# Kernel tuning notes

Hardware: AMD Instinct MI355X
Metric: run time of the kernel (lower is better)

The kernel has to match this reference:

```python
import jax, jax.numpy as jnp
import numpy as np

N = 100000   # num nodes
E = 1600000  # num edges (before self-loops)
D_IN, D_HID, D_OUT = 128, 128, 64


def _gcn_layer(x, W, b, src, dst, norm):
    # GCNConv: h = x @ W, then normalized sparse aggregation, then bias.
    h = x @ W                              # [N, d_out]
    msg = h[src] * norm[:, None]           # [E+N, d_out] gathered + scaled messages
    out = jax.ops.segment_sum(msg, dst, num_segments=N)  # scatter-add to dst nodes
    return out + b


def reference(x, W1, b1, W2, b2, edge_index):
    src0, dst0 = edge_index[0], edge_index[1]
    # GCNConv adds self-loops by default
    loop = jnp.arange(N, dtype=src0.dtype)
    src = jnp.concatenate([src0, loop])
    dst = jnp.concatenate([dst0, loop])
    # symmetric normalization: deg^{-1/2}[src] * deg^{-1/2}[dst]
    deg = jax.ops.segment_sum(jnp.ones_like(src, dtype=x.dtype), dst, num_segments=N)
    dinv = jnp.where(deg > 0, jax.lax.rsqrt(jnp.maximum(deg, 1.0)), 0.0)
    norm = dinv[src] * dinv[dst]           # [E+N]

    h = jax.nn.relu(_gcn_layer(x, W1, b1, src, dst, norm))
    return _gcn_layer(h, W2, b2, src, dst, norm)


def setup_inputs() -> dict:
    key = jax.random.key(0)
    k1, k2, k3, k4 = jax.random.split(key, 4)
    x = jax.random.normal(k1, (N, D_IN), dtype=jnp.float32)
    # glorot-ish init for weights
    W1 = jax.random.normal(k2, (D_IN, D_HID), dtype=jnp.float32) * (1.0 / np.sqrt(D_IN))
    b1 = jnp.zeros((D_HID,), dtype=jnp.float32)
    W2 = jax.random.normal(k3, (D_HID, D_OUT), dtype=jnp.float32) * (1.0 / np.sqrt(D_HID))
    b2 = jnp.zeros((D_OUT,), dtype=jnp.float32)
    edge_index = jax.random.randint(k4, (2, E), 0, N, dtype=jnp.int64)
    return {"x": x, "W1": W1, "b1": b1, "W2": W2, "b2": b2, "edge_index": edge_index}
```

## Files before the change

kernel.cpp:

```cpp
#include <hip/hip_runtime.h>

static constexpr int NN = 100000;
static constexpr int EE = 1600000;
static constexpr int BSZ = 64;
static constexpr int NB = (NN + BSZ - 1) / BSZ;
static constexpr int BCAP = 2048;
static constexpr int TILE = 2048;


__device__ __forceinline__ unsigned short f2bf(float f) {
    unsigned u = __float_as_uint(f);
    u += 0x7FFFu + ((u >> 16) & 1u);
    return (unsigned short)(u >> 16);
}
__device__ __forceinline__ float bfl(unsigned u) { return __uint_as_float(u << 16); }
__device__ __forceinline__ float bfh(unsigned u) { return __uint_as_float(u & 0xFFFF0000u); }

typedef __attribute__((ext_vector_type(8))) short short8;
typedef __attribute__((ext_vector_type(4))) float float4v;


__global__ __launch_bounds__(256) void k_init(const float* __restrict__ W1,
                                              const float* __restrict__ W2,
                                              unsigned short* __restrict__ W1t,
                                              unsigned short* __restrict__ W2t,
                                              int* __restrict__ bcur) {
    int idx = blockIdx.x * 256 + threadIdx.x;
    if (idx < 16384) {
        int n = idx >> 7, k = idx & 127;
        W1t[idx] = f2bf(W1[k * 128 + n]);
    } else if (idx < 24576) {
        int j = idx - 16384;
        int n = j >> 7, k = j & 127;
        W2t[j] = f2bf(W2[k * 64 + n]);
    } else if (idx < 24576 + NB) {
        int b = idx - 24576;
        bcur[b] = b * BCAP;
    }
}


__global__ __launch_bounds__(256) void k_bin(const int* __restrict__ src,
                                             const int* __restrict__ dst,
                                             int* __restrict__ bcur,
                                             int* __restrict__ ebuf, int E) {
    constexpr int K = TILE / 256;
    __shared__ int lcnt[NB];
    __shared__ int lbase[NB];
    const int t = threadIdx.x;
    const int e0 = blockIdx.x * TILE;

    for (int i = t; i < NB; i += 256) lcnt[i] = 0;
    __syncthreads();

    int dreg[K], ofs[K];
#pragma unroll
    for (int k = 0; k < K; ++k) {
        int e = e0 + k * 256 + t;
        if (e < E) {
            int d = dst[e];
            dreg[k] = d;
            ofs[k] = atomicAdd(&lcnt[d >> 6], 1);
        } else dreg[k] = -1;
    }
    __syncthreads();

    for (int i = t; i < NB; i += 256) {
        int c = lcnt[i];
        lbase[i] = c ? atomicAdd(&bcur[i], c) : 0;
    }
    __syncthreads();

#pragma unroll
    for (int k = 0; k < K; ++k) {
        if (dreg[k] >= 0) {
            int e = e0 + k * 256 + t;
            int s = src[e];
            int b = dreg[k] >> 6;
            ebuf[lbase[b] + ofs[k]] = (s << 6) | (dreg[k] & 63);
        }
    }
}


__global__ __launch_bounds__(256) void k_csr(const int* __restrict__ bcur,
                                             const int* __restrict__ ebuf,
                                             int* __restrict__ rowbeg,
                                             int* __restrict__ rowend,
                                             float* __restrict__ dinv,
                                             int* __restrict__ csr, int n) {
    __shared__ int lcnt[BSZ];
    __shared__ int lofs[BSZ];
    const int b = blockIdx.x, t = threadIdx.x;
    if (t < BSZ) lcnt[t] = 0;
    __syncthreads();
    const int beg = b * BCAP, end = bcur[b];
    for (int j = beg + t; j < end; j += 256) atomicAdd(&lcnt[ebuf[j] & 63], 1);
    __syncthreads();
    if (t < BSZ) {
        int c = lcnt[t];
        int x = c;
#pragma unroll
        for (int off = 1; off < 64; off <<= 1) {
            int y = __shfl_up(x, off, 64);
            if (t >= off) x += y;
        }
        int exc = x - c;
        int node = b * BSZ + t;
        if (node < n) {
            rowbeg[node] = beg + exc;
            rowend[node] = beg + exc + c;
            dinv[node] = rsqrtf((float)c + 1.0f);
        }
        lofs[t] = beg + exc;
    }
    __syncthreads();
    for (int j = beg + t; j < end; j += 256) {
        int e = ebuf[j];
        int pos = atomicAdd(&lofs[e & 63], 1);
        csr[pos] = e >> 6;
    }
}


__global__ __launch_bounds__(256) void k_gemm128m(const float* __restrict__ X,
                                                  const unsigned short* __restrict__ W1t,
                                                  const float* __restrict__ dinv,
                                                  unsigned* __restrict__ G, int M) {
    __shared__ float cls[4 * 16 * 132];
    const int t = threadIdx.x;
    const int w = t >> 6, lane = t & 63;
    const int quad = lane >> 4, m16 = lane & 15;
    const int row0 = blockIdx.x * 64 + w * 16;
    int arow = row0 + m16; if (arow >= M) arow = M - 1;

    short8 afrag[4];
#pragma unroll
    for (int ks = 0; ks < 4; ++ks) {
        const float* p = X + (size_t)arow * 128 + ks * 32 + quad * 8;
        float4 u0 = ((const float4*)p)[0];
        float4 u1 = ((const float4*)p)[1];
        short8 a;
        a[0] = (short)f2bf(u0.x); a[1] = (short)f2bf(u0.y);
        a[2] = (short)f2bf(u0.z); a[3] = (short)f2bf(u0.w);
        a[4] = (short)f2bf(u1.x); a[5] = (short)f2bf(u1.y);
        a[6] = (short)f2bf(u1.z); a[7] = (short)f2bf(u1.w);
        afrag[ks] = a;
    }
    float* myc = cls + w * 16 * 132;
#pragma unroll
    for (int nt = 0; nt < 8; ++nt) {
        float4v acc = {0.f, 0.f, 0.f, 0.f};
#pragma unroll
        for (int ks = 0; ks < 4; ++ks) {
            const short8 b = *((const short8*)(W1t + (size_t)(nt * 16 + m16) * 128 + ks * 32 + quad * 8));
            acc = __builtin_amdgcn_mfma_f32_16x16x32_bf16(afrag[ks], b, acc, 0, 0, 0);
        }
#pragma unroll
        for (int r = 0; r < 4; ++r)
            myc[(quad * 4 + r) * 132 + nt * 16 + m16] = acc[r];
    }
    __syncthreads();
#pragma unroll
    for (int i = 0; i < 8; ++i) {
        int idx = i * 64 + lane;
        int r = idx >> 5, c = idx & 31;
        int grow = row0 + r;
        if (grow < M) {
            float4 v = *((const float4*)(myc + r * 132 + c * 4));
            float s = dinv[grow];
            uint2 p;
            p.x = (unsigned)f2bf(v.x * s) | ((unsigned)f2bf(v.y * s) << 16);
            p.y = (unsigned)f2bf(v.z * s) | ((unsigned)f2bf(v.w * s) << 16);
            ((uint2*)G)[(size_t)grow * 32 + c] = p;
        }
    }
}


__global__ __launch_bounds__(256) void k_gemm64m(const unsigned short* __restrict__ X,
                                                 const unsigned short* __restrict__ W2t,
                                                 const float* __restrict__ dinv,
                                                 unsigned* __restrict__ G, int M) {
    __shared__ float cls[4 * 16 * 68];
    const int t = threadIdx.x;
    const int w = t >> 6, lane = t & 63;
    const int quad = lane >> 4, m16 = lane & 15;
    const int row0 = blockIdx.x * 64 + w * 16;
    int arow = row0 + m16; if (arow >= M) arow = M - 1;

    short8 afrag[4];
#pragma unroll
    for (int ks = 0; ks < 4; ++ks)
        afrag[ks] = *((const short8*)(X + (size_t)arow * 128 + ks * 32 + quad * 8));

    float* myc = cls + w * 16 * 68;
#pragma unroll
    for (int nt = 0; nt < 4; ++nt) {
        float4v acc = {0.f, 0.f, 0.f, 0.f};
#pragma unroll
        for (int ks = 0; ks < 4; ++ks) {
            const short8 b = *((const short8*)(W2t + (size_t)(nt * 16 + m16) * 128 + ks * 32 + quad * 8));
            acc = __builtin_amdgcn_mfma_f32_16x16x32_bf16(afrag[ks], b, acc, 0, 0, 0);
        }
#pragma unroll
        for (int r = 0; r < 4; ++r)
            myc[(quad * 4 + r) * 68 + nt * 16 + m16] = acc[r];
    }
    __syncthreads();
#pragma unroll
    for (int i = 0; i < 4; ++i) {
        int idx = i * 64 + lane;
        int r = idx >> 4, c = idx & 15;
        int grow = row0 + r;
        if (grow < M) {
            float4 v = *((const float4*)(myc + r * 68 + c * 4));
            float s = dinv[grow];
            uint2 p;
            p.x = (unsigned)f2bf(v.x * s) | ((unsigned)f2bf(v.y * s) << 16);
            p.y = (unsigned)f2bf(v.z * s) | ((unsigned)f2bf(v.w * s) << 16);
            ((uint2*)G)[(size_t)grow * 16 + c] = p;
        }
    }
}


__global__ __launch_bounds__(256) void k_gather128(const int* __restrict__ rowbeg,
                                                   const int* __restrict__ rowend,
                                                   const int* __restrict__ csr,
                                                   const unsigned* __restrict__ G,
                                                   const float* __restrict__ dinv,
                                                   const float* __restrict__ bias,
                                                   unsigned* __restrict__ OUT,
                                                   int n, int nwaves) {
    const int wid = blockIdx.x * 4 + (threadIdx.x >> 6);
    const int lane = threadIdx.x & 63;
    const int sub = lane & 31;
    const int half = lane >> 5;
    for (int node = wid; node < n; node += nwaves) {
        const int beg = rowbeg[node];
        const int end = rowend[node];
        float a0 = 0.f, a1 = 0.f, a2 = 0.f, a3 = 0.f;
        for (int c = beg; c < end; c += 64) {
            int ec = end - c; if (ec > 64) ec = 64;
            const int idx = csr[c + ((lane < ec) ? lane : 0)];
            int pb = 0;
            for (; pb + 16 <= ec; pb += 16) {
#pragma unroll
                for (int q = 0; q < 8; ++q) {
                    int s = __shfl(idx, pb + 2 * q + half, 64);
                    uint2 v = *((const uint2*)(G + (size_t)s * 64 + 2 * sub));
                    a0 += bfl(v.x); a1 += bfh(v.x); a2 += bfl(v.y); a3 += bfh(v.y);
                }
            }
            if (pb < ec) {
#pragma unroll
                for (int q = 0; q < 8; ++q) {
                    int e = pb + 2 * q + half;
                    bool valid = e < ec;
                    int s = __shfl(idx, valid ? e : 0, 64);
                    uint2 v = *((const uint2*)(G + (size_t)s * 64 + 2 * sub));
                    if (valid) { a0 += bfl(v.x); a1 += bfh(v.x); a2 += bfl(v.y); a3 += bfh(v.y); }
                }
            }
        }
        a0 += __shfl_xor(a0, 32, 64);
        a1 += __shfl_xor(a1, 32, 64);
        a2 += __shfl_xor(a2, 32, 64);
        a3 += __shfl_xor(a3, 32, 64);
        if (half == 0) {
            uint2 vs = *((const uint2*)(G + (size_t)node * 64 + 2 * sub));
            a0 += bfl(vs.x); a1 += bfh(vs.x); a2 += bfl(vs.y); a3 += bfh(vs.y);
            const float di = dinv[node];
            const float4 bv = ((const float4*)bias)[sub];
            float r0 = fmaf(a0, di, bv.x), r1 = fmaf(a1, di, bv.y);
            float r2 = fmaf(a2, di, bv.z), r3 = fmaf(a3, di, bv.w);
            r0 = fmaxf(r0, 0.f); r1 = fmaxf(r1, 0.f);
            r2 = fmaxf(r2, 0.f); r3 = fmaxf(r3, 0.f);
            uint2 p;
            p.x = (unsigned)f2bf(r0) | ((unsigned)f2bf(r1) << 16);
            p.y = (unsigned)f2bf(r2) | ((unsigned)f2bf(r3) << 16);
            ((uint2*)OUT)[(size_t)node * 32 + sub] = p;
        }
    }
}


__global__ __launch_bounds__(256) void k_gather64(const int* __restrict__ rowbeg,
                                                  const int* __restrict__ rowend,
                                                  const int* __restrict__ csr,
                                                  const unsigned* __restrict__ G,
                                                  const float* __restrict__ dinv,
                                                  const float* __restrict__ bias,
                                                  float* __restrict__ OUT,
                                                  int n, int nwaves) {
    const int wid = blockIdx.x * 4 + (threadIdx.x >> 6);
    const int lane = threadIdx.x & 63;
    const int sub = lane & 15;
    const int qh = lane >> 4;
    for (int node = wid; node < n; node += nwaves) {
        const int beg = rowbeg[node];
        const int end = rowend[node];
        float a0 = 0.f, a1 = 0.f, a2 = 0.f, a3 = 0.f;
        for (int c = beg; c < end; c += 64) {
            int ec = end - c; if (ec > 64) ec = 64;
            const int idx = csr[c + ((lane < ec) ? lane : 0)];
            int pb = 0;
            for (; pb + 32 <= ec; pb += 32) {
#pragma unroll
                for (int q = 0; q < 8; ++q) {
                    int s = __shfl(idx, pb + 4 * q + qh, 64);
                    uint2 v = ((const uint2*)(G + (size_t)s * 32))[sub];
                    a0 += bfl(v.x); a1 += bfh(v.x); a2 += bfl(v.y); a3 += bfh(v.y);
                }
            }
            if (pb < ec) {
#pragma unroll
                for (int q = 0; q < 8; ++q) {
                    int e = pb + 4 * q + qh;
                    bool valid = e < ec;
                    int s = __shfl(idx, valid ? e : 0, 64);
                    uint2 v = ((const uint2*)(G + (size_t)s * 32))[sub];
                    if (valid) { a0 += bfl(v.x); a1 += bfh(v.x); a2 += bfl(v.y); a3 += bfh(v.y); }
                }
            }
        }
        a0 += __shfl_xor(a0, 16, 64); a0 += __shfl_xor(a0, 32, 64);
        a1 += __shfl_xor(a1, 16, 64); a1 += __shfl_xor(a1, 32, 64);
        a2 += __shfl_xor(a2, 16, 64); a2 += __shfl_xor(a2, 32, 64);
        a3 += __shfl_xor(a3, 16, 64); a3 += __shfl_xor(a3, 32, 64);
        if (qh == 0) {
            uint2 vs = ((const uint2*)(G + (size_t)node * 32))[sub];
            a0 += bfl(vs.x); a1 += bfh(vs.x); a2 += bfl(vs.y); a3 += bfh(vs.y);
            const float di = dinv[node];
            const float4 bv = ((const float4*)bias)[sub];
            float4 r;
            r.x = fmaf(a0, di, bv.x);
            r.y = fmaf(a1, di, bv.y);
            r.z = fmaf(a2, di, bv.z);
            r.w = fmaf(a3, di, bv.w);
            ((float4*)OUT)[(size_t)node * 16 + sub] = r;
        }
    }
}


extern "C" void kernel_launch(void* const* d_in, const int* in_sizes, int n_in,
                              void* d_out, int out_size, void* d_ws, size_t ws_size,
                              hipStream_t stream) {
    const float* x  = (const float*)d_in[0];
    const float* W1 = (const float*)d_in[1];
    const float* b1 = (const float*)d_in[2];
    const float* W2 = (const float*)d_in[3];
    const float* b2 = (const float*)d_in[4];
    const int*   ei = (const int*)d_in[5];
    const int* src = ei;
    const int* dst = ei + EE;
    float* out = (float*)d_out;

    int*   bcur   = (int*)d_ws;
    float* dinv   = (float*)(bcur + NB);
    int*   rowbeg = (int*)(dinv + NN);
    int*   rowend = rowbeg + NN;
    int*   ebuf   = rowend + NN;
    int*   csr    = ebuf + (size_t)NB * BCAP;
    unsigned* g1b = (unsigned*)(csr + (size_t)NB * BCAP);
    unsigned* h1b = g1b + (size_t)NN * 64;
    unsigned* g2b = h1b + (size_t)NN * 64;
    unsigned short* w1t = (unsigned short*)(g2b + (size_t)NN * 32);
    unsigned short* w2t = w1t + 16384;

    constexpr int GB = 2048;
    constexpr int NW = GB * 4;
    constexpr int IB = (24576 + NB + 255) / 256;

    k_init<<<IB, 256, 0, stream>>>(W1, W2, w1t, w2t, bcur);
    k_bin<<<(EE + TILE - 1) / TILE, 256, 0, stream>>>(src, dst, bcur, ebuf, EE);
    k_csr<<<NB, 256, 0, stream>>>(bcur, ebuf, rowbeg, rowend, dinv, csr, NN);

    k_gemm128m<<<(NN + 63) / 64, 256, 0, stream>>>(x, w1t, dinv, g1b, NN);
    k_gather128<<<GB, 256, 0, stream>>>(rowbeg, rowend, csr, g1b, dinv, b1, h1b, NN, NW);

    k_gemm64m<<<(NN + 63) / 64, 256, 0, stream>>>((const unsigned short*)h1b, w2t, dinv, g2b, NN);
    k_gather64<<<GB, 256, 0, stream>>>(rowbeg, rowend, csr, g2b, dinv, b2, out, NN, NW);
}
```

Measured before the change: 345.6 us.

## Slice feature matrices into column slabs and gather per slab for cache locality

Intermediate feature matrices G1, H1 and G2 are stored as column slabs of 16 features (NN x 16 bf16 each), and the GEMM epilogues and A-operand loads are rewritten to match. A single templated gather kernel assigns blocks to one slab, so each wave gathers 32-byte rows from a slab small enough to stay in cache, with 4 nodes per wave and 16 edges per step. Row begin and end are packed into an int2, with nontemporal loads and stores and software prefetch of the next node's CSR indices. The cost is that the csr list is read once per slice (8 or 4 times), plus more complex indexing.

```diff
diff --git a/kernel.cpp b/kernel.cpp
--- a/kernel.cpp
+++ b/kernel.cpp
@@ -6,6 +6,7 @@
 static constexpr int NB = (NN + BSZ - 1) / BSZ;
 static constexpr int BCAP = 2048;
 static constexpr int TILE = 2048;
+static constexpr int GB = 2048;
 
 
 __device__ __forceinline__ unsigned short f2bf(float f) {
@@ -18,6 +19,7 @@
 
 typedef __attribute__((ext_vector_type(8))) short short8;
 typedef __attribute__((ext_vector_type(4))) float float4v;
+typedef __attribute__((ext_vector_type(4))) float float4n;
 
 
 __global__ __launch_bounds__(256) void k_init(const float* __restrict__ W1,
@@ -85,8 +87,7 @@
 
 __global__ __launch_bounds__(256) void k_csr(const int* __restrict__ bcur,
                                              const int* __restrict__ ebuf,
-                                             int* __restrict__ rowbeg,
-                                             int* __restrict__ rowend,
+                                             int2* __restrict__ rbe,
                                              float* __restrict__ dinv,
                                              int* __restrict__ csr, int n) {
     __shared__ int lcnt[BSZ];
@@ -108,8 +109,7 @@
         int exc = x - c;
         int node = b * BSZ + t;
         if (node < n) {
-            rowbeg[node] = beg + exc;
-            rowend[node] = beg + exc + c;
+            rbe[node] = make_int2(beg + exc, beg + exc + c);
             dinv[node] = rsqrtf((float)c + 1.0f);
         }
         lofs[t] = beg + exc;
@@ -172,7 +172,7 @@
             uint2 p;
             p.x = (unsigned)f2bf(v.x * s) | ((unsigned)f2bf(v.y * s) << 16);
             p.y = (unsigned)f2bf(v.z * s) | ((unsigned)f2bf(v.w * s) << 16);
-            ((uint2*)G)[(size_t)grow * 32 + c] = p;
+            ((uint2*)G)[(size_t)(c >> 2) * NN * 4 + (size_t)grow * 4 + (c & 3)] = p;
         }
     }
 }
@@ -191,8 +191,10 @@
 
     short8 afrag[4];
 #pragma unroll
-    for (int ks = 0; ks < 4; ++ks)
-        afrag[ks] = *((const short8*)(X + (size_t)arow * 128 + ks * 32 + quad * 8));
+    for (int ks = 0; ks < 4; ++ks) {
+        const int slab = 2 * ks + (quad >> 1);
+        afrag[ks] = *((const short8*)(X + (size_t)slab * NN * 16 + (size_t)arow * 16 + (quad & 1) * 8));
+    }
 
     float* myc = cls + w * 16 * 68;
 #pragma unroll
@@ -219,127 +221,103 @@
             uint2 p;
             p.x = (unsigned)f2bf(v.x * s) | ((unsigned)f2bf(v.y * s) << 16);
             p.y = (unsigned)f2bf(v.z * s) | ((unsigned)f2bf(v.w * s) << 16);
-            ((uint2*)G)[(size_t)grow * 16 + c] = p;
-        }
-    }
-}
-
-
-__global__ __launch_bounds__(256) void k_gather128(const int* __restrict__ rowbeg,
-                                                   const int* __restrict__ rowend,
-                                                   const int* __restrict__ csr,
-                                                   const unsigned* __restrict__ G,
-                                                   const float* __restrict__ dinv,
-                                                   const float* __restrict__ bias,
-                                                   unsigned* __restrict__ OUT,
-                                                   int n, int nwaves) {
-    const int wid = blockIdx.x * 4 + (threadIdx.x >> 6);
+            ((uint2*)G)[(size_t)(c >> 2) * NN * 4 + (size_t)grow * 4 + (c & 3)] = p;
+        }
+    }
+}
+
+
+__device__ __forceinline__ int2 ld_rbe(const int2* __restrict__ rbe, int node, int n) {
+    int2 r = make_int2(0, 0);
+    if (node < n) {
+        long long v = __builtin_nontemporal_load((const long long*)(rbe + node));
+        r.x = (int)(v & 0xffffffffll);
+        r.y = (int)(v >> 32);
+    }
+    return r;
+}
+__device__ __forceinline__ int ld_csr(const int* __restrict__ csr, int2 re, int off) {
+    int deg = re.y - re.x;
+    int v = __builtin_nontemporal_load(csr + re.x + ((off < deg) ? off : 0));
+    return (deg > 0) ? v : 0;
+}
+
+template<int LAYER>
+__global__ __launch_bounds__(256) void k_gather_s(
+        const int2* __restrict__ rbe, const int* __restrict__ csr,
+        const unsigned* __restrict__ Gall, const float* __restrict__ dinv,
+        const float* __restrict__ bias, unsigned* __restrict__ OUT, int n) {
     const int lane = threadIdx.x & 63;
-    const int sub = lane & 31;
-    const int half = lane >> 5;
-    for (int node = wid; node < n; node += nwaves) {
-        const int beg = rowbeg[node];
-        const int end = rowend[node];
+    const int w = threadIdx.x >> 6;
+    const int q = lane >> 4;
+    const int l16 = lane & 15;
+    const int g4 = (lane >> 2) & 3;
+    const int sub = lane & 3;
+    const int shbase = (lane & 48) | g4;
+
+    int slice, wis, stride;
+    if (LAYER == 1) {
+        slice = blockIdx.x & 7;
+        wis = (blockIdx.x >> 3) * 4 + w;
+        stride = (GB / 8) * 4;
+    } else {
+        slice = (blockIdx.x & 7) >> 1;
+        wis = (blockIdx.x >> 3) * 8 + (blockIdx.x & 1) * 4 + w;
+        stride = (GB / 8) * 8;
+    }
+    const int iter_nodes = stride * 4;
+    const uint2* slab = (const uint2*)(Gall + (size_t)slice * NN * 8);
+
+    int node = wis * 4 + q;
+    int2 re_cur = ld_rbe(rbe, node, n);
+    int2 re_nx  = ld_rbe(rbe, node + iter_nodes, n);
+    int idx_cur = ld_csr(csr, re_cur, l16);
+
+    for (; node < n; node += iter_nodes) {
+        const int2 re = re_cur;
+        int idx = idx_cur;
+        re_cur = re_nx;
+        re_nx  = ld_rbe(rbe, node + 2 * iter_nodes, n);
+        idx_cur = ld_csr(csr, re_cur, l16);
+
+        const int deg = re.y - re.x;
         float a0 = 0.f, a1 = 0.f, a2 = 0.f, a3 = 0.f;
-        for (int c = beg; c < end; c += 64) {
-            int ec = end - c; if (ec > 64) ec = 64;
-            const int idx = csr[c + ((lane < ec) ? lane : 0)];
-            int pb = 0;
-            for (; pb + 16 <= ec; pb += 16) {
-#pragma unroll
-                for (int q = 0; q < 8; ++q) {
-                    int s = __shfl(idx, pb + 2 * q + half, 64);
-                    uint2 v = *((const uint2*)(G + (size_t)s * 64 + 2 * sub));
-                    a0 += bfl(v.x); a1 += bfh(v.x); a2 += bfl(v.y); a3 += bfh(v.y);
-                }
+        for (int eo = 0; eo < BCAP; ) {
+#pragma unroll
+            for (int st = 0; st < 4; ++st) {
+                int e = eo + st * 4 + g4;
+                int s = __shfl(idx, shbase | (st << 2), 64);
+                uint2 v = slab[(size_t)s * 4 + sub];
+                if (e < deg) { a0 += bfl(v.x); a1 += bfh(v.x); a2 += bfl(v.y); a3 += bfh(v.y); }
             }
-            if (pb < ec) {
-#pragma unroll
-                for (int q = 0; q < 8; ++q) {
-                    int e = pb + 2 * q + half;
-                    bool valid = e < ec;
-                    int s = __shfl(idx, valid ? e : 0, 64);
-                    uint2 v = *((const uint2*)(G + (size_t)s * 64 + 2 * sub));
-                    if (valid) { a0 += bfl(v.x); a1 += bfh(v.x); a2 += bfl(v.y); a3 += bfh(v.y); }
-                }
-            }
-        }
-        a0 += __shfl_xor(a0, 32, 64);
-        a1 += __shfl_xor(a1, 32, 64);
-        a2 += __shfl_xor(a2, 32, 64);
-        a3 += __shfl_xor(a3, 32, 64);
-        if (half == 0) {
-            uint2 vs = *((const uint2*)(G + (size_t)node * 64 + 2 * sub));
+            eo += 16;
+            if (!__any(eo < deg)) break;
+            idx = ld_csr(csr, re, eo + l16);
+        }
+        a0 += __shfl_xor(a0, 4, 64); a0 += __shfl_xor(a0, 8, 64);
+        a1 += __shfl_xor(a1, 4, 64); a1 += __shfl_xor(a1, 8, 64);
+        a2 += __shfl_xor(a2, 4, 64); a2 += __shfl_xor(a2, 8, 64);
+        a3 += __shfl_xor(a3, 4, 64); a3 += __shfl_xor(a3, 8, 64);
+        if (g4 == 0) {
+            uint2 vs = slab[(size_t)node * 4 + sub];
             a0 += bfl(vs.x); a1 += bfh(vs.x); a2 += bfl(vs.y); a3 += bfh(vs.y);
             const float di = dinv[node];
-            const float4 bv = ((const float4*)bias)[sub];
+            const float4 bv = ((const float4*)bias)[slice * 4 + sub];
             float r0 = fmaf(a0, di, bv.x), r1 = fmaf(a1, di, bv.y);
             float r2 = fmaf(a2, di, bv.z), r3 = fmaf(a3, di, bv.w);
-            r0 = fmaxf(r0, 0.f); r1 = fmaxf(r1, 0.f);
-            r2 = fmaxf(r2, 0.f); r3 = fmaxf(r3, 0.f);
-            uint2 p;
-            p.x = (unsigned)f2bf(r0) | ((unsigned)f2bf(r1) << 16);
-            p.y = (unsigned)f2bf(r2) | ((unsigned)f2bf(r3) << 16);
-            ((uint2*)OUT)[(size_t)node * 32 + sub] = p;
-        }
-    }
-}
-
-
-__global__ __launch_bounds__(256) void k_gather64(const int* __restrict__ rowbeg,
-                                                  const int* __restrict__ rowend,
-                                                  const int* __restrict__ csr,
-                                                  const unsigned* __restrict__ G,
-                                                  const float* __restrict__ dinv,
-                                                  const float* __restrict__ bias,
-                                                  float* __restrict__ OUT,
-                                                  int n, int nwaves) {
-    const int wid = blockIdx.x * 4 + (threadIdx.x >> 6);
-    const int lane = threadIdx.x & 63;
-    const int sub = lane & 15;
-    const int qh = lane >> 4;
-    for (int node = wid; node < n; node += nwaves) {
-        const int beg = rowbeg[node];
-        const int end = rowend[node];
-        float a0 = 0.f, a1 = 0.f, a2 = 0.f, a3 = 0.f;
-        for (int c = beg; c < end; c += 64) {
-            int ec = end - c; if (ec > 64) ec = 64;
-            const int idx = csr[c + ((lane < ec) ? lane : 0)];
-            int pb = 0;
-            for (; pb + 32 <= ec; pb += 32) {
-#pragma unroll
-                for (int q = 0; q < 8; ++q) {
-                    int s = __shfl(idx, pb + 4 * q + qh, 64);
-                    uint2 v = ((const uint2*)(G + (size_t)s * 32))[sub];
-                    a0 += bfl(v.x); a1 += bfh(v.x); a2 += bfl(v.y); a3 += bfh(v.y);
-                }
+            if (LAYER == 1) {
+                r0 = fmaxf(r0, 0.f); r1 = fmaxf(r1, 0.f);
+                r2 = fmaxf(r2, 0.f); r3 = fmaxf(r3, 0.f);
+                unsigned lo = (unsigned)f2bf(r0) | ((unsigned)f2bf(r1) << 16);
+                unsigned hi = (unsigned)f2bf(r2) | ((unsigned)f2bf(r3) << 16);
+                unsigned long long p = (unsigned long long)lo | ((unsigned long long)hi << 32);
+                __builtin_nontemporal_store(p,
+                    (unsigned long long*)((uint2*)OUT + (size_t)slice * NN * 4 + (size_t)node * 4 + sub));
+            } else {
+                float4n r = {r0, r1, r2, r3};
+                __builtin_nontemporal_store(r,
+                    (float4n*)OUT + (size_t)node * 16 + slice * 4 + sub);
             }
-            if (pb < ec) {
-#pragma unroll
-                for (int q = 0; q < 8; ++q) {
-                    int e = pb + 4 * q + qh;
-                    bool valid = e < ec;
-                    int s = __shfl(idx, valid ? e : 0, 64);
-                    uint2 v = ((const uint2*)(G + (size_t)s * 32))[sub];
-                    if (valid) { a0 += bfl(v.x); a1 += bfh(v.x); a2 += bfl(v.y); a3 += bfh(v.y); }
-                }
-            }
-        }
-        a0 += __shfl_xor(a0, 16, 64); a0 += __shfl_xor(a0, 32, 64);
-        a1 += __shfl_xor(a1, 16, 64); a1 += __shfl_xor(a1, 32, 64);
-        a2 += __shfl_xor(a2, 16, 64); a2 += __shfl_xor(a2, 32, 64);
-        a3 += __shfl_xor(a3, 16, 64); a3 += __shfl_xor(a3, 32, 64);
-        if (qh == 0) {
-            uint2 vs = ((const uint2*)(G + (size_t)node * 32))[sub];
-            a0 += bfl(vs.x); a1 += bfh(vs.x); a2 += bfl(vs.y); a3 += bfh(vs.y);
-            const float di = dinv[node];
-            const float4 bv = ((const float4*)bias)[sub];
-            float4 r;
-            r.x = fmaf(a0, di, bv.x);
-            r.y = fmaf(a1, di, bv.y);
-            r.z = fmaf(a2, di, bv.z);
-            r.w = fmaf(a3, di, bv.w);
-            ((float4*)OUT)[(size_t)node * 16 + sub] = r;
         }
     }
 }
@@ -358,29 +336,26 @@
     const int* dst = ei + EE;
     float* out = (float*)d_out;
 
-    int*   bcur   = (int*)d_ws;
-    float* dinv   = (float*)(bcur + NB);
-    int*   rowbeg = (int*)(dinv + NN);
-    int*   rowend = rowbeg + NN;
-    int*   ebuf   = rowend + NN;
-    int*   csr    = ebuf + (size_t)NB * BCAP;
-    unsigned* g1b = (unsigned*)(csr + (size_t)NB * BCAP);
+    unsigned* g1b = (unsigned*)d_ws;
     unsigned* h1b = g1b + (size_t)NN * 64;
     unsigned* g2b = h1b + (size_t)NN * 64;
     unsigned short* w1t = (unsigned short*)(g2b + (size_t)NN * 32);
     unsigned short* w2t = w1t + 16384;
-
-    constexpr int GB = 2048;
-    constexpr int NW = GB * 4;
+    int2*  rbe  = (int2*)(w2t + 8192);
+    float* dinv = (float*)(rbe + NN);
+    int*   bcur = (int*)(dinv + NN);
+    int*   ebuf = bcur + NB;
+    int*   csr  = ebuf + (size_t)NB * BCAP;
+
     constexpr int IB = (24576 + NB + 255) / 256;
 
     k_init<<<IB, 256, 0, stream>>>(W1, W2, w1t, w2t, bcur);
     k_bin<<<(EE + TILE - 1) / TILE, 256, 0, stream>>>(src, dst, bcur, ebuf, EE);
-    k_csr<<<NB, 256, 0, stream>>>(bcur, ebuf, rowbeg, rowend, dinv, csr, NN);
+    k_csr<<<NB, 256, 0, stream>>>(bcur, ebuf, rbe, dinv, csr, NN);
 
     k_gemm128m<<<(NN + 63) / 64, 256, 0, stream>>>(x, w1t, dinv, g1b, NN);
-    k_gather128<<<GB, 256, 0, stream>>>(rowbeg, rowend, csr, g1b, dinv, b1, h1b, NN, NW);
+    k_gather_s<1><<<GB, 256, 0, stream>>>(rbe, csr, g1b, dinv, b1, h1b, NN);
 
     k_gemm64m<<<(NN + 63) / 64, 256, 0, stream>>>((const unsigned short*)h1b, w2t, dinv, g2b, NN);
-    k_gather64<<<GB, 256, 0, stream>>>(rowbeg, rowend, csr, g2b, dinv, b2, out, NN, NW);
-}
+    k_gather_s<2><<<GB, 256, 0, stream>>>(rbe, csr, g2b, dinv, b2, (unsigned*)out, NN);
+}
```

Result: slower. 420.9 us (+21.8%).

## Build CSR via global degree count, scan, and atomic fill

Applied to the files above, without the earlier changes.

Replaces the two-pass bucketed binning (per-block LDS histogram into 64-node buckets, then per-bucket local sort) with a classic CSR build: global atomic degree count, two-kernel prefix scan, and an atomic-cursor fill of source indices. This removes the fixed-capacity bucket buffer and its per-bucket overflow risk, and gives a compact CSR. In exchange it issues 1.6M global atomics twice on random destinations and scatters csr writes randomly, where the old approach wrote mostly coalesced runs. Within-row edge order becomes nondeterministic.

```diff
diff --git a/kernel.cpp b/kernel.cpp
--- a/kernel.cpp
+++ b/kernel.cpp
@@ -2,10 +2,9 @@
 
 static constexpr int NN = 100000;
 static constexpr int EE = 1600000;
-static constexpr int BSZ = 64;
-static constexpr int NB = (NN + BSZ - 1) / BSZ;
-static constexpr int BCAP = 2048;
-static constexpr int TILE = 2048;
+static constexpr int GB = 2048;
+static constexpr int SB = 512;
+static constexpr int NBS = (NN + SB - 1) / SB;
 
 
 __device__ __forceinline__ unsigned short f2bf(float f) {
@@ -24,7 +23,7 @@
                                               const float* __restrict__ W2,
                                               unsigned short* __restrict__ W1t,
                                               unsigned short* __restrict__ W2t,
-                                              int* __restrict__ bcur) {
+                                              int* __restrict__ deg) {
     int idx = blockIdx.x * 256 + threadIdx.x;
     if (idx < 16384) {
         int n = idx >> 7, k = idx & 127;
@@ -33,92 +32,96 @@
         int j = idx - 16384;
         int n = j >> 7, k = j & 127;
         W2t[j] = f2bf(W2[k * 64 + n]);
-    } else if (idx < 24576 + NB) {
-        int b = idx - 24576;
-        bcur[b] = b * BCAP;
-    }
-}
-
-
-__global__ __launch_bounds__(256) void k_bin(const int* __restrict__ src,
-                                             const int* __restrict__ dst,
-                                             int* __restrict__ bcur,
-                                             int* __restrict__ ebuf, int E) {
-    constexpr int K = TILE / 256;
-    __shared__ int lcnt[NB];
-    __shared__ int lbase[NB];
-    const int t = threadIdx.x;
-    const int e0 = blockIdx.x * TILE;
-
-    for (int i = t; i < NB; i += 256) lcnt[i] = 0;
-    __syncthreads();
-
-    int dreg[K], ofs[K];
-#pragma unroll
-    for (int k = 0; k < K; ++k) {
-        int e = e0 + k * 256 + t;
-        if (e < E) {
-            int d = dst[e];
-            dreg[k] = d;
-            ofs[k] = atomicAdd(&lcnt[d >> 6], 1);
-        } else dreg[k] = -1;
-    }
-    __syncthreads();
-
-    for (int i = t; i < NB; i += 256) {
-        int c = lcnt[i];
-        lbase[i] = c ? atomicAdd(&bcur[i], c) : 0;
-    }
-    __syncthreads();
-
-#pragma unroll
-    for (int k = 0; k < K; ++k) {
-        if (dreg[k] >= 0) {
-            int e = e0 + k * 256 + t;
-            int s = src[e];
-            int b = dreg[k] >> 6;
-            ebuf[lbase[b] + ofs[k]] = (s << 6) | (dreg[k] & 63);
-        }
-    }
-}
-
-
-__global__ __launch_bounds__(256) void k_csr(const int* __restrict__ bcur,
-                                             const int* __restrict__ ebuf,
-                                             int* __restrict__ rowbeg,
-                                             int* __restrict__ rowend,
-                                             float* __restrict__ dinv,
-                                             int* __restrict__ csr, int n) {
-    __shared__ int lcnt[BSZ];
-    __shared__ int lofs[BSZ];
-    const int b = blockIdx.x, t = threadIdx.x;
-    if (t < BSZ) lcnt[t] = 0;
-    __syncthreads();
-    const int beg = b * BCAP, end = bcur[b];
-    for (int j = beg + t; j < end; j += 256) atomicAdd(&lcnt[ebuf[j] & 63], 1);
-    __syncthreads();
-    if (t < BSZ) {
-        int c = lcnt[t];
-        int x = c;
-#pragma unroll
-        for (int off = 1; off < 64; off <<= 1) {
-            int y = __shfl_up(x, off, 64);
-            if (t >= off) x += y;
-        }
-        int exc = x - c;
-        int node = b * BSZ + t;
-        if (node < n) {
-            rowbeg[node] = beg + exc;
-            rowend[node] = beg + exc + c;
-            dinv[node] = rsqrtf((float)c + 1.0f);
-        }
-        lofs[t] = beg + exc;
-    }
-    __syncthreads();
-    for (int j = beg + t; j < end; j += 256) {
-        int e = ebuf[j];
-        int pos = atomicAdd(&lofs[e & 63], 1);
-        csr[pos] = e >> 6;
+    } else if (idx < 24576 + NN) {
+        deg[idx - 24576] = 0;
+    }
+}
+
+
+__global__ __launch_bounds__(256) void k_deg(const int* __restrict__ dst,
+                                             int* __restrict__ deg, int E) {
+    const int stride = gridDim.x * 256;
+    for (int e = blockIdx.x * 256 + threadIdx.x; e < E; e += stride)
+        atomicAdd(&deg[dst[e]], 1);
+}
+
+
+__global__ __launch_bounds__(SB) void k_scan1(const int* __restrict__ deg,
+                                              int* __restrict__ bsum) {
+    const int t = threadIdx.x, lane = t & 63, wid = t >> 6;
+    int i = blockIdx.x * SB + t;
+    int v = (i < NN) ? deg[i] : 0;
+#pragma unroll
+    for (int off = 1; off < 64; off <<= 1) v += __shfl_xor(v, off, 64);
+    __shared__ int ws[SB / 64];
+    if (lane == 0) ws[wid] = v;
+    __syncthreads();
+    if (t == 0) {
+        int s = 0;
+#pragma unroll
+        for (int k = 0; k < SB / 64; ++k) s += ws[k];
+        bsum[blockIdx.x] = s;
+    }
+}
+
+
+__global__ __launch_bounds__(SB) void k_scan3(const int* __restrict__ deg,
+                                              const int* __restrict__ bsum,
+                                              int* __restrict__ rowbeg,
+                                              int* __restrict__ rowend,
+                                              int* __restrict__ cur,
+                                              float* __restrict__ dinv) {
+    const int b = blockIdx.x, t = threadIdx.x, lane = t & 63, wid = t >> 6;
+    int v = (t < b) ? bsum[t] : 0;
+#pragma unroll
+    for (int off = 1; off < 64; off <<= 1) v += __shfl_xor(v, off, 64);
+    __shared__ int ws[SB / 64];
+    __shared__ int sbase;
+    if (lane == 0) ws[wid] = v;
+    __syncthreads();
+    if (t == 0) {
+        int s = 0;
+#pragma unroll
+        for (int k = 0; k < SB / 64; ++k) s += ws[k];
+        sbase = s;
+    }
+    int i = b * SB + t;
+    int d = (i < NN) ? deg[i] : 0;
+    int x = d;
+#pragma unroll
+    for (int off = 1; off < 64; off <<= 1) {
+        int y = __shfl_up(x, off, 64);
+        if (lane >= off) x += y;
+    }
+    __shared__ int wsum[SB / 64];
+    __shared__ int wexc[SB / 64];
+    if (lane == 63) wsum[wid] = x;
+    __syncthreads();
+    if (t == 0) {
+        int s = 0;
+#pragma unroll
+        for (int k = 0; k < SB / 64; ++k) { wexc[k] = s; s += wsum[k]; }
+    }
+    __syncthreads();
+    int excl = sbase + wexc[wid] + x - d;
+    if (i < NN) {
+        rowbeg[i] = excl;
+        rowend[i] = excl + d;
+        cur[i]    = excl;
+        dinv[i]   = rsqrtf((float)d + 1.0f);
+    }
+}
+
+
+__global__ __launch_bounds__(256) void k_fill(const int* __restrict__ src,
+                                              const int* __restrict__ dst,
+                                              int* __restrict__ cur,
+                                              int* __restrict__ csr, int E) {
+    const int stride = gridDim.x * 256;
+    for (int e = blockIdx.x * 256 + threadIdx.x; e < E; e += stride) {
+        int s = src[e], d = dst[e];
+        int pos = atomicAdd(&cur[d], 1);
+        csr[pos] = s;
     }
 }
 
@@ -358,29 +361,32 @@
     const int* dst = ei + EE;
     float* out = (float*)d_out;
 
-    int*   bcur   = (int*)d_ws;
-    float* dinv   = (float*)(bcur + NB);
-    int*   rowbeg = (int*)(dinv + NN);
-    int*   rowend = rowbeg + NN;
-    int*   ebuf   = rowend + NN;
-    int*   csr    = ebuf + (size_t)NB * BCAP;
-    unsigned* g1b = (unsigned*)(csr + (size_t)NB * BCAP);
-    unsigned* h1b = g1b + (size_t)NN * 64;
-    unsigned* g2b = h1b + (size_t)NN * 64;
-    unsigned short* w1t = (unsigned short*)(g2b + (size_t)NN * 32);
-    unsigned short* w2t = w1t + 16384;
-
-    constexpr int GB = 2048;
-    constexpr int NW = GB * 4;
-    constexpr int IB = (24576 + NB + 255) / 256;
-
-    k_init<<<IB, 256, 0, stream>>>(W1, W2, w1t, w2t, bcur);
-    k_bin<<<(EE + TILE - 1) / TILE, 256, 0, stream>>>(src, dst, bcur, ebuf, EE);
-    k_csr<<<NB, 256, 0, stream>>>(bcur, ebuf, rowbeg, rowend, dinv, csr, NN);
+    char* p = (char*)d_ws;
+    unsigned* g1b = (unsigned*)p;             p += (size_t)NN * 64 * 4;
+    unsigned* h1b = (unsigned*)p;             p += (size_t)NN * 64 * 4;
+    unsigned* g2b = (unsigned*)p;             p += (size_t)NN * 32 * 4;
+    unsigned short* w1t = (unsigned short*)p; p += 16384 * 2;
+    unsigned short* w2t = (unsigned short*)p; p += 8192 * 2;
+    int*   deg    = (int*)p;                  p += (size_t)NN * 4;
+    int*   rowbeg = (int*)p;                  p += (size_t)NN * 4;
+    int*   rowend = (int*)p;                  p += (size_t)NN * 4;
+    int*   cur    = (int*)p;                  p += (size_t)NN * 4;
+    float* dinv   = (float*)p;                p += (size_t)NN * 4;
+    int*   bsum   = (int*)p;                  p += ((size_t)NBS * 4 + 15) & ~(size_t)15;
+    int*   csr    = (int*)p;                  p += (size_t)EE * 4;
+
+    constexpr int NWG = GB * 4;
+    constexpr int IB = (24576 + NN + 255) / 256;
+
+    k_init<<<IB, 256, 0, stream>>>(W1, W2, w1t, w2t, deg);
+    k_deg<<<2048, 256, 0, stream>>>(dst, deg, EE);
+    k_scan1<<<NBS, SB, 0, stream>>>(deg, bsum);
+    k_scan3<<<NBS, SB, 0, stream>>>(deg, bsum, rowbeg, rowend, cur, dinv);
+    k_fill<<<2048, 256, 0, stream>>>(src, dst, cur, csr, EE);
 
     k_gemm128m<<<(NN + 63) / 64, 256, 0, stream>>>(x, w1t, dinv, g1b, NN);
-    k_gather128<<<GB, 256, 0, stream>>>(rowbeg, rowend, csr, g1b, dinv, b1, h1b, NN, NW);
+    k_gather128<<<GB, 256, 0, stream>>>(rowbeg, rowend, csr, g1b, dinv, b1, h1b, NN, NWG);
 
     k_gemm64m<<<(NN + 63) / 64, 256, 0, stream>>>((const unsigned short*)h1b, w2t, dinv, g2b, NN);
-    k_gather64<<<GB, 256, 0, stream>>>(rowbeg, rowend, csr, g2b, dinv, b2, out, NN, NW);
-}
+    k_gather64<<<GB, 256, 0, stream>>>(rowbeg, rowend, csr, g2b, dinv, b2, out, NN, NWG);
+}
```

New measurement: 455.6 us. 31.8% more time.
